# Performance work log

Hardware: AMD Instinct MI355X
Metric: run time of the kernel (lower is better)

The kernel has to match this reference:

```python
import jax, jax.numpy as jnp
import numpy as np

N, E, D, G, S, H = 100000, 1600000, 64, 1024, 4096, 128
BN_EPS = 1e-5


def setup_inputs() -> dict:
    key = jax.random.key(0)
    ks = jax.random.split(key, 24)
    x = jax.random.normal(ks[0], (N, D), jnp.float32)
    sid = jax.random.randint(ks[1], (N,), 0, S)
    x = x.at[:, 5].set(sid.astype(jnp.float32))  # column 5 holds integer substructure ids
    edge_index = jax.random.randint(ks[2], (2, E), 0, N, dtype=jnp.int32)
    batch = jnp.sort(jax.random.randint(ks[3], (N,), 0, G, dtype=jnp.int32))

    def lin(k, fan_in, shape):
        return jax.random.normal(k, shape, jnp.float32) / np.sqrt(fan_in)

    return {
        "x": x, "edge_index": edge_index, "batch": batch,
        # substructure attention net: Linear(D,64) -> tanh -> Linear(64,1,no bias)
        "w1": lin(ks[4], D, (D, 64)), "b1": jnp.zeros((64,), jnp.float32),
        "w2": lin(ks[5], 64, (64,)),
        "cw0": lin(ks[6], D + 1, (D + 1, H)), "cb0": jnp.zeros((H,), jnp.float32),
        "cw_rest": lin(ks[7], H, (3, H, H)), "cb_rest": jnp.zeros((3, H), jnp.float32),
        # BatchNorm1d (eval mode: running stats)
        "bn_gamma": jnp.ones((4, H), jnp.float32), "bn_beta": jnp.zeros((4, H), jnp.float32),
        "bn_mean": 0.1 * jax.random.normal(ks[8], (4, H), jnp.float32),
        "bn_var": jax.random.uniform(ks[9], (4, H), jnp.float32, 0.5, 1.5),
        # pred head: Linear(128,64) -> ELU -> Linear(64,1)
        "hw1": lin(ks[10], H, (H, 64)), "hb1": jnp.zeros((64,), jnp.float32),
        "hw2": lin(ks[11], 64, (64, 1)), "hb2": jnp.zeros((1,), jnp.float32),
    }


def _subst_attention(x, subst_ids, w1, b1, w2):
    ones = jnp.ones((x.shape[0],), x.dtype)
    cnt = jax.ops.segment_sum(ones, subst_ids, num_segments=S)
    sums = jax.ops.segment_sum(x, subst_ids, num_segments=S)
    means = sums / jnp.maximum(cnt, 1.0)[:, None]          # [S, D] per-substructure mean
    scores = jnp.tanh(means @ w1 + b1) @ w2                # [S]
    attn = jax.nn.softmax(scores, axis=0)                  # softmax over substructures
    return attn[subst_ids][:, None]                        # [N, 1] broadcast back to atoms


def _gcn(x, W, b, row, col, norm, n):
    h = x @ W                                              # [N, H]
    msg = h[row] * norm[:, None]                           # gather + scale  [E+N, H]
    return jax.ops.segment_sum(msg, col, num_segments=n) + b


def reference(x, edge_index, batch, w1, b1, w2, cw0, cb0, cw_rest, cb_rest,
              bn_gamma, bn_beta, bn_mean, bn_var, hw1, hb1, hw2, hb2):
    n = x.shape[0]
    subst_ids = jax.lax.stop_gradient(x[:, 5]).astype(jnp.int32)
    attn = _subst_attention(x, subst_ids, w1, b1, w2)
    h = jnp.concatenate([x, attn], axis=1)                 # [N, D+1]

    # add self loops, symmetric GCN normalization (as in PyG GCNConv)
    loops = jnp.arange(n, dtype=edge_index.dtype)
    row = jnp.concatenate([edge_index[0], loops])
    col = jnp.concatenate([edge_index[1], loops])
    deg = jax.ops.segment_sum(jnp.ones_like(row, dtype=h.dtype), col, num_segments=n)
    dinv = jax.lax.rsqrt(jnp.maximum(deg, 1.0))
    norm = dinv[row] * dinv[col]

    def bn(z, i):
        return (z - bn_mean[i]) * jax.lax.rsqrt(bn_var[i] + BN_EPS) * bn_gamma[i] + bn_beta[i]

    h = jax.nn.elu(bn(_gcn(h, cw0, cb0, row, col, norm, n), 0))
    for i in range(3):
        z = bn(_gcn(h, cw_rest[i], cb_rest[i], row, col, norm, n), i + 1)
        h = jax.nn.elu(z) if i < 2 else jax.nn.relu(z)

    # global mean pool over graphs
    gcnt = jax.ops.segment_sum(jnp.ones((n,), h.dtype), batch, num_segments=G)
    pooled = jax.ops.segment_sum(h, batch, num_segments=G) / jnp.maximum(gcnt, 1.0)[:, None]

    return jax.nn.elu(pooled @ hw1 + hb1) @ hw2 + hb2      # [G, 1]
```

## Files before the change

kernel.cpp:

```cpp
#include <hip/hip_runtime.h>
#include <math.h>

static constexpr int SS = 4096;
static constexpr int HH = 128;
static constexpr float EPS_BN = 1e-5f;

typedef __attribute__((ext_vector_type(8))) short bf16x8;
typedef __attribute__((ext_vector_type(4))) float f32x4;

__device__ inline unsigned short f2bf(float f) {
  unsigned int u = __float_as_uint(f);
  return (unsigned short)((u + 0x7fffu + ((u >> 16) & 1u)) >> 16);
}
__device__ inline float bflo(unsigned int u) { return __uint_as_float(u << 16); }
__device__ inline float bfhi(unsigned int u) { return __uint_as_float(u & 0xffff0000u); }


__global__ __launch_bounds__(256)
void gcn_front1(const int* __restrict__ col, int* __restrict__ fill, int* __restrict__ pos,
                const float* __restrict__ x, float* __restrict__ cnt, float* __restrict__ sums,
                int n, int e, int nbPos) {
  int b = blockIdx.x;
  int t = threadIdx.x;
  if (b < nbPos) {
    int i = b * 256 + t;
    if (i < e) pos[i] = atomicAdd(&fill[col[i]], 1);
    return;
  }
  b -= nbPos;
  {
    int node = b * 4 + (t >> 6);
    int lane = t & 63;
    if (node >= n) return;
    const float* xr = x + (size_t)node * 64;
    float v = xr[lane];
    int sid = (int)__shfl(v, 5, 64);
    if (lane == 0) atomicAdd(&cnt[sid], 1.0f);
    atomicAdd(&sums[(size_t)sid * 64 + lane], v);
  }
}


__global__ void gcn_scores(const float* __restrict__ sums, const float* __restrict__ cnt,
                           const float* __restrict__ w1, const float* __restrict__ b1,
                           const float* __restrict__ w2, float* __restrict__ scores) {
  int s = blockIdx.x * 4 + (threadIdx.x >> 6);
  int j = threadIdx.x & 63;
  float r = 1.0f / fmaxf(cnt[s], 1.0f);
  const float* ss = sums + (size_t)s * 64;
  float acc = b1[j];
  #pragma unroll 8
  for (int d = 0; d < 64; ++d) acc = fmaf(ss[d] * r, w1[d * 64 + j], acc);
  float t = tanhf(acc) * w2[j];
  #pragma unroll
  for (int off = 32; off; off >>= 1) t += __shfl_down(t, off, 64);
  if (j == 0) scores[s] = t;
}

__global__ void gcn_softmax(float* __restrict__ sc) {
  int t = threadIdx.x;
  int wid = t >> 6;
  float v[4]; float m = -INFINITY;
  for (int i = 0; i < 4; ++i) { v[i] = sc[t + i * 1024]; m = fmaxf(m, v[i]); }
  for (int off = 32; off; off >>= 1) m = fmaxf(m, __shfl_xor(m, off, 64));
  __shared__ float wmax[16];
  if ((t & 63) == 0) wmax[wid] = m;
  __syncthreads();
  if (t == 0) { float mm = wmax[0]; for (int i = 1; i < 16; ++i) mm = fmaxf(mm, wmax[i]); wmax[0] = mm; }
  __syncthreads();
  float M = wmax[0];
  float s = 0.f;
  for (int i = 0; i < 4; ++i) { v[i] = expf(v[i] - M); s += v[i]; }
  for (int off = 32; off; off >>= 1) s += __shfl_xor(s, off, 64);
  __shared__ float wsum[16];
  if ((t & 63) == 0) wsum[wid] = s;
  __syncthreads();
  if (t == 0) { float ts = 0.f; for (int i = 0; i < 16; ++i) ts += wsum[i]; wsum[0] = ts; }
  __syncthreads();
  float inv = 1.0f / wsum[0];
  for (int i = 0; i < 4; ++i) sc[t + i * 1024] = v[i] * inv;
}


__global__ void gcn_scan1(const int* __restrict__ fill, int* __restrict__ rowstart,
                          int* __restrict__ bsum, float* __restrict__ dinv, int n) {
  __shared__ int tmp[1024];
  int t = threadIdx.x; int g = blockIdx.x * 1024 + t;
  int v = (g < n) ? fill[g] : 0;
  if (g < n) dinv[g] = rsqrtf((float)v + 1.0f);
  tmp[t] = v; __syncthreads();
  for (int off = 1; off < 1024; off <<= 1) {
    int a = (t >= off) ? tmp[t - off] : 0; __syncthreads();
    tmp[t] += a; __syncthreads();
  }
  if (g < n) rowstart[g] = tmp[t] - v;
  if (t == 1023) bsum[blockIdx.x] = tmp[t];
}

__global__ void gcn_scan2(int* __restrict__ bsum, int nb) {
  __shared__ int tmp[128];
  int t = threadIdx.x;
  int v = (t < nb) ? bsum[t] : 0;
  tmp[t] = v; __syncthreads();
  for (int off = 1; off < 128; off <<= 1) {
    int a = (t >= off) ? tmp[t - off] : 0; __syncthreads();
    tmp[t] += a; __syncthreads();
  }
  if (t < nb) bsum[t] = tmp[t] - v;
}

__global__ void gcn_scan3(int* __restrict__ rowstart, const int* __restrict__ bsum, int n, int e) {
  int g = blockIdx.x * 1024 + threadIdx.x;
  if (g < n) rowstart[g] += bsum[blockIdx.x];
  if (g == 0) rowstart[n] = e;
}


__device__ void wpack_body(const float* __restrict__ W, unsigned short* __restrict__ out,
                           int nkc, int idx) {
  if (idx >= 8 * nkc * 64) return;
  int lane = idx & 63;
  int kc = (idx >> 6) % nkc;
  int nt = idx / (64 * nkc);
  int colc = nt * 16 + (lane & 15);
  int k0 = kc * 32 + (lane >> 4) * 8;
  unsigned int w[4];
  #pragma unroll
  for (int i = 0; i < 4; ++i) {
    unsigned short a = f2bf(W[(size_t)(k0 + 2 * i) * 128 + colc]);
    unsigned short b = f2bf(W[(size_t)(k0 + 2 * i + 1) * 128 + colc]);
    w[i] = (unsigned int)a | ((unsigned int)b << 16);
  }
  *(uint4*)&out[(size_t)idx * 8] = make_uint4(w[0], w[1], w[2], w[3]);
}

__global__ __launch_bounds__(256)
void gcn_front3(const float* __restrict__ x, const float* __restrict__ attn,
                float2* __restrict__ np,
                const int* __restrict__ row, const int* __restrict__ col,
                const int* __restrict__ pos, const int* __restrict__ rowstart,
                const float* __restrict__ dinv, int2* __restrict__ sedge,
                unsigned int* __restrict__ xh, const int* __restrict__ batch,
                int* __restrict__ gstart,
                const float* __restrict__ cw0, const float* __restrict__ cwr,
                unsigned short* __restrict__ wpk0, unsigned short* __restrict__ wpkr,
                const float* __restrict__ cb0, const float* __restrict__ cbr,
                const float* __restrict__ bng, const float* __restrict__ bnb,
                const float* __restrict__ bnm, const float* __restrict__ bnv,
                float* __restrict__ bnS, float* __restrict__ bnT,
                int n, int e, int G,
                int nbSc, int nbNp, int nbXb, int nbGb, int nbW0, int nbWr) {
  int b = blockIdx.x;
  int t = threadIdx.x;
  if (b < nbSc) {
    int i = b * 256 + t;
    if (i >= e) return;
    int c = col[i], r = row[i];
    sedge[rowstart[c] + pos[i]] = make_int2(r, __float_as_int(dinv[r] * dinv[c]));
    return;
  }
  b -= nbSc;
  if (b < nbNp) {
    int i = b * 256 + t;
    if (i >= n) return;
    int sid = (int)x[(size_t)i * 64 + 5];
    np[i] = make_float2((float)sid, attn[sid]);
    return;
  }
  b -= nbNp;
  if (b < nbXb) {
    int i = b * 256 + t;
    if (i >= n * 32) return;
    int pr = i & 31;
    float2 v = *(const float2*)&x[(size_t)(i >> 5) * 64 + pr * 2];
    if (pr == 2) v.y = 0.f;
    xh[i] = (unsigned int)f2bf(v.x) | ((unsigned int)f2bf(v.y) << 16);
    return;
  }
  b -= nbXb;
  if (b < nbGb) {
    int g = b * 256 + t;
    if (g > G) return;
    if (g == G) { gstart[G] = n; return; }
    int lo = 0, hi = n;
    while (lo < hi) { int mid = (lo + hi) >> 1; if (batch[mid] < g) lo = mid + 1; else hi = mid; }
    gstart[g] = lo;
    return;
  }
  b -= nbGb;
  if (b < nbW0) { wpack_body(cw0, wpk0, 2, b * 256 + t); return; }
  b -= nbW0;
  if (b < 3 * nbWr) {
    int l = b / nbWr, bb = b % nbWr;
    wpack_body(cwr + (size_t)l * HH * HH, wpkr + (size_t)l * 8 * 4 * 64 * 8, 4, bb * 256 + t);
    return;
  }
  b -= 3 * nbWr;
  {
    int i = b * 256 + t;
    if (i >= 512) return;
    int l = i >> 7, c = i & 127;
    float S = rsqrtf(bnv[i] + EPS_BN) * bng[i];
    float bias = (l == 0) ? cb0[c] : cbr[(l - 1) * 128 + c];
    bnS[i] = S;
    bnT[i] = fmaf(bias - bnm[i], S, bnb[i]);
  }
}


__global__ __launch_bounds__(256)
void gcn_layer_f(const unsigned short* __restrict__ hIn, const int2* __restrict__ sedge,
                 const int* __restrict__ rowstart, const float* __restrict__ dinv,
                 const unsigned short* __restrict__ Wpk,
                 const float* __restrict__ bnS, const float* __restrict__ bnT,
                 unsigned short* __restrict__ hOut, int relu, int n) {
  __shared__ unsigned short tile[4][16][136];
  int t = threadIdx.x;
  int wid = t >> 6, l = t & 63;
  int r = l & 15, kg = l >> 4;
  size_t row0w = (size_t)blockIdx.x * 64 + wid * 16;
  int noderaw = (int)row0w + r;
  bool valid = noderaw < n;
  int node = valid ? noderaw : n - 1;
  float di = dinv[node], d2 = di * di;
  const uint4* h4 = (const uint4*)hIn;
  float a[4][8];
  #pragma unroll
  for (int kc = 0; kc < 4; ++kc) {
    uint4 u = h4[(size_t)node * 16 + kc * 4 + kg];
    a[kc][0] = bflo(u.x) * d2; a[kc][1] = bfhi(u.x) * d2;
    a[kc][2] = bflo(u.y) * d2; a[kc][3] = bfhi(u.y) * d2;
    a[kc][4] = bflo(u.z) * d2; a[kc][5] = bfhi(u.z) * d2;
    a[kc][6] = bflo(u.w) * d2; a[kc][7] = bfhi(u.w) * d2;
  }
  int s_ = valid ? rowstart[node] : 0;
  int e_ = valid ? rowstart[node + 1] : 0;
  int j = s_;
  for (; j + 2 <= e_; j += 2) {
    int2 sA = sedge[j], sB = sedge[j + 1];
    float wA = __int_as_float(sA.y), wB = __int_as_float(sB.y);
    uint4 uA[4], uB[4];
    #pragma unroll
    for (int kc = 0; kc < 4; ++kc) uA[kc] = h4[(size_t)sA.x * 16 + kc * 4 + kg];
    #pragma unroll
    for (int kc = 0; kc < 4; ++kc) uB[kc] = h4[(size_t)sB.x * 16 + kc * 4 + kg];
    #pragma unroll
    for (int kc = 0; kc < 4; ++kc) {
      a[kc][0] = fmaf(bflo(uA[kc].x), wA, a[kc][0]); a[kc][1] = fmaf(bfhi(uA[kc].x), wA, a[kc][1]);
      a[kc][2] = fmaf(bflo(uA[kc].y), wA, a[kc][2]); a[kc][3] = fmaf(bfhi(uA[kc].y), wA, a[kc][3]);
      a[kc][4] = fmaf(bflo(uA[kc].z), wA, a[kc][4]); a[kc][5] = fmaf(bfhi(uA[kc].z), wA, a[kc][5]);
      a[kc][6] = fmaf(bflo(uA[kc].w), wA, a[kc][6]); a[kc][7] = fmaf(bfhi(uA[kc].w), wA, a[kc][7]);
    }
    #pragma unroll
    for (int kc = 0; kc < 4; ++kc) {
      a[kc][0] = fmaf(bflo(uB[kc].x), wB, a[kc][0]); a[kc][1] = fmaf(bfhi(uB[kc].x), wB, a[kc][1]);
      a[kc][2] = fmaf(bflo(uB[kc].y), wB, a[kc][2]); a[kc][3] = fmaf(bfhi(uB[kc].y), wB, a[kc][3]);
      a[kc][4] = fmaf(bflo(uB[kc].z), wB, a[kc][4]); a[kc][5] = fmaf(bfhi(uB[kc].z), wB, a[kc][5]);
      a[kc][6] = fmaf(bflo(uB[kc].w), wB, a[kc][6]); a[kc][7] = fmaf(bfhi(uB[kc].w), wB, a[kc][7]);
    }
  }
  if (j < e_) {
    int2 sA = sedge[j];
    float wA = __int_as_float(sA.y);
    #pragma unroll
    for (int kc = 0; kc < 4; ++kc) {
      uint4 u = h4[(size_t)sA.x * 16 + kc * 4 + kg];
      a[kc][0] = fmaf(bflo(u.x), wA, a[kc][0]); a[kc][1] = fmaf(bfhi(u.x), wA, a[kc][1]);
      a[kc][2] = fmaf(bflo(u.y), wA, a[kc][2]); a[kc][3] = fmaf(bfhi(u.y), wA, a[kc][3]);
      a[kc][4] = fmaf(bflo(u.z), wA, a[kc][4]); a[kc][5] = fmaf(bfhi(u.z), wA, a[kc][5]);
      a[kc][6] = fmaf(bflo(u.w), wA, a[kc][6]); a[kc][7] = fmaf(bfhi(u.w), wA, a[kc][7]);
    }
  }
  bf16x8 af[4];
  #pragma unroll
  for (int kc = 0; kc < 4; ++kc) {
    uint4 pk;
    pk.x = (unsigned)f2bf(a[kc][0]) | ((unsigned)f2bf(a[kc][1]) << 16);
    pk.y = (unsigned)f2bf(a[kc][2]) | ((unsigned)f2bf(a[kc][3]) << 16);
    pk.z = (unsigned)f2bf(a[kc][4]) | ((unsigned)f2bf(a[kc][5]) << 16);
    pk.w = (unsigned)f2bf(a[kc][6]) | ((unsigned)f2bf(a[kc][7]) << 16);
    af[kc] = *(bf16x8*)&pk;
  }
  f32x4 acc[8];
  #pragma unroll
  for (int nt = 0; nt < 8; ++nt) acc[nt] = (f32x4){0.f, 0.f, 0.f, 0.f};
  const unsigned short* wp = Wpk + (size_t)l * 8;
  #pragma unroll
  for (int kc = 0; kc < 4; ++kc) {
    bf16x8 bf[8];
    #pragma unroll
    for (int nt = 0; nt < 8; ++nt)
      bf[nt] = *(const bf16x8*)(wp + (size_t)(nt * 4 + kc) * 512);
    #pragma unroll
    for (int nt = 0; nt < 8; ++nt)
      acc[nt] = __builtin_amdgcn_mfma_f32_16x16x32_bf16(af[kc], bf[nt], acc[nt], 0, 0, 0);
  }
  int colb = l & 15, rb = kg * 4;
  #pragma unroll
  for (int nt = 0; nt < 8; ++nt) {
    int c = nt * 16 + colb;
    float S = bnS[c], T = bnT[c];
    #pragma unroll
    for (int jj = 0; jj < 4; ++jj) {
      float v = fmaf(acc[nt][jj], S, T);
      v = relu ? fmaxf(v, 0.f) : (v > 0.f ? v : expf(v) - 1.f);
      tile[wid][rb + jj][c] = f2bf(v);
    }
  }
  __syncthreads();
  #pragma unroll
  for (int i = 0; i < 4; ++i) {
    int m = i * 64 + l;
    int rr = m >> 4, chunk = m & 15;
    uint4 v = *(const uint4*)&tile[wid][rr][chunk * 8];
    *(uint4*)&hOut[(row0w + rr) * 128 + chunk * 8] = v;
  }
}


__global__ __launch_bounds__(256)
void gcn_layer0_f(const unsigned int* __restrict__ xh, const float2* __restrict__ np,
                  const int2* __restrict__ sedge, const int* __restrict__ rowstart,
                  const float* __restrict__ dinv, const unsigned short* __restrict__ Wpk0,
                  const float* __restrict__ cw0,
                  const float* __restrict__ bnS, const float* __restrict__ bnT,
                  unsigned short* __restrict__ hOut, int n) {
  __shared__ unsigned short tile[4][16][136];
  int t = threadIdx.x;
  int wid = t >> 6, l = t & 63;
  int r = l & 15, kg = l >> 4;
  size_t row0w = (size_t)blockIdx.x * 64 + wid * 16;
  int noderaw = (int)row0w + r;
  bool valid = noderaw < n;
  int node = valid ? noderaw : n - 1;
  float di = dinv[node], d2 = di * di;
  const uint4* x4 = (const uint4*)xh;
  float a[2][8];
  #pragma unroll
  for (int kc = 0; kc < 2; ++kc) {
    uint4 u = x4[(size_t)node * 8 + kc * 4 + kg];
    a[kc][0] = bflo(u.x) * d2; a[kc][1] = bfhi(u.x) * d2;
    a[kc][2] = bflo(u.y) * d2; a[kc][3] = bfhi(u.y) * d2;
    a[kc][4] = bflo(u.z) * d2; a[kc][5] = bfhi(u.z) * d2;
    a[kc][6] = bflo(u.w) * d2; a[kc][7] = bfhi(u.w) * d2;
  }
  float a5 = 0.f, a64 = 0.f;
  if (kg == 0) { float2 v = np[node]; a5 = d2 * v.x; a64 = d2 * v.y; }
  int s_ = valid ? rowstart[node] : 0;
  int e_ = valid ? rowstart[node + 1] : 0;
  int j = s_;
  for (; j + 2 <= e_; j += 2) {
    int2 sA = sedge[j], sB = sedge[j + 1];
    float wA = __int_as_float(sA.y), wB = __int_as_float(sB.y);
    uint4 uA[2], uB[2];
    #pragma unroll
    for (int kc = 0; kc < 2; ++kc) uA[kc] = x4[(size_t)sA.x * 8 + kc * 4 + kg];
    #pragma unroll
    for (int kc = 0; kc < 2; ++kc) uB[kc] = x4[(size_t)sB.x * 8 + kc * 4 + kg];
    float2 vA, vB;
    if (kg == 0) { vA = np[sA.x]; vB = np[sB.x]; }
    #pragma unroll
    for (int kc = 0; kc < 2; ++kc) {
      a[kc][0] = fmaf(bflo(uA[kc].x), wA, a[kc][0]); a[kc][1] = fmaf(bfhi(uA[kc].x), wA, a[kc][1]);
      a[kc][2] = fmaf(bflo(uA[kc].y), wA, a[kc][2]); a[kc][3] = fmaf(bfhi(uA[kc].y), wA, a[kc][3]);
      a[kc][4] = fmaf(bflo(uA[kc].z), wA, a[kc][4]); a[kc][5] = fmaf(bfhi(uA[kc].z), wA, a[kc][5]);
      a[kc][6] = fmaf(bflo(uA[kc].w), wA, a[kc][6]); a[kc][7] = fmaf(bfhi(uA[kc].w), wA, a[kc][7]);
      a[kc][0] = fmaf(bflo(uB[kc].x), wB, a[kc][0]); a[kc][1] = fmaf(bfhi(uB[kc].x), wB, a[kc][1]);
      a[kc][2] = fmaf(bflo(uB[kc].y), wB, a[kc][2]); a[kc][3] = fmaf(bfhi(uB[kc].y), wB, a[kc][3]);
      a[kc][4] = fmaf(bflo(uB[kc].z), wB, a[kc][4]); a[kc][5] = fmaf(bfhi(uB[kc].z), wB, a[kc][5]);
      a[kc][6] = fmaf(bflo(uB[kc].w), wB, a[kc][6]); a[kc][7] = fmaf(bfhi(uB[kc].w), wB, a[kc][7]);
    }
    if (kg == 0) {
      a5 = fmaf(vA.x, wA, a5); a64 = fmaf(vA.y, wA, a64);
      a5 = fmaf(vB.x, wB, a5); a64 = fmaf(vB.y, wB, a64);
    }
  }
  if (j < e_) {
    int2 sA = sedge[j];
    float wA = __int_as_float(sA.y);
    #pragma unroll
    for (int kc = 0; kc < 2; ++kc) {
      uint4 u = x4[(size_t)sA.x * 8 + kc * 4 + kg];
      a[kc][0] = fmaf(bflo(u.x), wA, a[kc][0]); a[kc][1] = fmaf(bfhi(u.x), wA, a[kc][1]);
      a[kc][2] = fmaf(bflo(u.y), wA, a[kc][2]); a[kc][3] = fmaf(bfhi(u.y), wA, a[kc][3]);
      a[kc][4] = fmaf(bflo(u.z), wA, a[kc][4]); a[kc][5] = fmaf(bfhi(u.z), wA, a[kc][5]);
      a[kc][6] = fmaf(bflo(u.w), wA, a[kc][6]); a[kc][7] = fmaf(bfhi(u.w), wA, a[kc][7]);
    }
    if (kg == 0) {
      float2 v = np[sA.x];
      a5 = fmaf(v.x, wA, a5); a64 = fmaf(v.y, wA, a64);
    }
  }
  bf16x8 af[2];
  #pragma unroll
  for (int kc = 0; kc < 2; ++kc) {
    uint4 pk;
    pk.x = (unsigned)f2bf(a[kc][0]) | ((unsigned)f2bf(a[kc][1]) << 16);
    pk.y = (unsigned)f2bf(a[kc][2]) | ((unsigned)f2bf(a[kc][3]) << 16);
    pk.z = (unsigned)f2bf(a[kc][4]) | ((unsigned)f2bf(a[kc][5]) << 16);
    pk.w = (unsigned)f2bf(a[kc][6]) | ((unsigned)f2bf(a[kc][7]) << 16);
    af[kc] = *(bf16x8*)&pk;
  }
  f32x4 acc[8];
  #pragma unroll
  for (int nt = 0; nt < 8; ++nt) acc[nt] = (f32x4){0.f, 0.f, 0.f, 0.f};
  const unsigned short* wp = Wpk0 + (size_t)l * 8;
  #pragma unroll
  for (int kc = 0; kc < 2; ++kc) {
    bf16x8 bf[8];
    #pragma unroll
    for (int nt = 0; nt < 8; ++nt)
      bf[nt] = *(const bf16x8*)(wp + (size_t)(nt * 2 + kc) * 512);
    #pragma unroll
    for (int nt = 0; nt < 8; ++nt)
      acc[nt] = __builtin_amdgcn_mfma_f32_16x16x32_bf16(af[kc], bf[nt], acc[nt], 0, 0, 0);
  }
  int colb = l & 15, rb = kg * 4;
  float2 ax[4];
  #pragma unroll
  for (int jj = 0; jj < 4; ++jj) {
    ax[jj].x = __shfl(a5, rb + jj, 64);
    ax[jj].y = __shfl(a64, rb + jj, 64);
  }
  #pragma unroll
  for (int nt = 0; nt < 8; ++nt) {
    int c = nt * 16 + colb;
    float w5 = cw0[5 * 128 + c], w64 = cw0[64 * 128 + c];
    float S = bnS[c], T = bnT[c];
    #pragma unroll
    for (int jj = 0; jj < 4; ++jj) {
      float z = acc[nt][jj] + ax[jj].x * w5 + ax[jj].y * w64;
      float v = fmaf(z, S, T);
      v = v > 0.f ? v : expf(v) - 1.f;
      tile[wid][rb + jj][c] = f2bf(v);
    }
  }
  __syncthreads();
  #pragma unroll
  for (int i = 0; i < 4; ++i) {
    int m = i * 64 + l;
    int rr = m >> 4, chunk = m & 15;
    uint4 v = *(const uint4*)&tile[wid][rr][chunk * 8];
    *(uint4*)&hOut[(row0w + rr) * 128 + chunk * 8] = v;
  }
}


__global__ __launch_bounds__(256)
void gcn_poolhead(const unsigned short* __restrict__ hB, const int* __restrict__ gstart,
                  const float* __restrict__ hw1, const float* __restrict__ hb1,
                  const float* __restrict__ hw2, const float* __restrict__ hb2,
                  float* __restrict__ out, int G) {
  __shared__ float pl[4][128];
  int wid = threadIdx.x >> 6, lane = threadIdx.x & 63;
  int g = blockIdx.x * 4 + wid;
  if (g >= G) return;
  int s = gstart[g], e = gstart[g + 1];
  const unsigned int* h32 = (const unsigned int*)hB;
  float ax = 0.f, ay = 0.f;
  int i = s;
  for (; i + 2 <= e; i += 2) {
    unsigned int u0 = h32[(size_t)i * 64 + lane];
    unsigned int u1 = h32[(size_t)(i + 1) * 64 + lane];
    ax += bflo(u0) + bflo(u1);
    ay += bfhi(u0) + bfhi(u1);
  }
  if (i < e) {
    unsigned int u = h32[(size_t)i * 64 + lane];
    ax += bflo(u); ay += bfhi(u);
  }
  float r = 1.0f / fmaxf((float)(e - s), 1.0f);
  pl[wid][lane * 2] = ax * r;
  pl[wid][lane * 2 + 1] = ay * r;
  float acc = hb1[lane];
  #pragma unroll 8
  for (int k = 0; k < 128; ++k) acc = fmaf(pl[wid][k], hw1[k * 64 + lane], acc);
  float t2 = acc > 0.f ? acc : expf(acc) - 1.f;
  t2 *= hw2[lane];
  #pragma unroll
  for (int off = 32; off; off >>= 1) t2 += __shfl_down(t2, off, 64);
  if (lane == 0) out[g] = t2 + hb2[0];
}


extern "C" void kernel_launch(void* const* d_in, const int* in_sizes, int n_in,
                              void* d_out, int out_size, void* d_ws, size_t ws_size,
                              hipStream_t stream) {
  const float* x   = (const float*)d_in[0];
  const int*   ei  = (const int*)d_in[1];
  const int*   batch = (const int*)d_in[2];
  const float* w1  = (const float*)d_in[3];
  const float* b1  = (const float*)d_in[4];
  const float* w2  = (const float*)d_in[5];
  const float* cw0 = (const float*)d_in[6];
  const float* cb0 = (const float*)d_in[7];
  const float* cwr = (const float*)d_in[8];
  const float* cbr = (const float*)d_in[9];
  const float* bng = (const float*)d_in[10];
  const float* bnb = (const float*)d_in[11];
  const float* bnm = (const float*)d_in[12];
  const float* bnv = (const float*)d_in[13];
  const float* hw1 = (const float*)d_in[14];
  const float* hb1 = (const float*)d_in[15];
  const float* hw2 = (const float*)d_in[16];
  const float* hb2 = (const float*)d_in[17];
  float* out = (float*)d_out;
  (void)n_in; (void)ws_size;

  const int n = in_sizes[0] / 64;
  const int e = in_sizes[1] / 2;
  const int G = out_size;
  const int* row = ei;
  const int* col = ei + e;
  const int nb128 = (n + 127) / 128;
  const int n_pad = nb128 * 128;

  char* p = (char*)d_ws;
  auto take = [&](size_t bytes) { char* r = p; p += (bytes + 255) & ~(size_t)255; return r; };
  float* cnt    = (float*)take((size_t)SS * 4);
  float* sums   = (float*)take((size_t)SS * 64 * 4);
  float* attn   = (float*)take((size_t)SS * 4);
  float* dinv   = (float*)take((size_t)n * 4);
  int*   rowst  = (int*)take(((size_t)n + 1) * 4);
  int*   fill   = (int*)take((size_t)n * 4);
  int*   pos    = (int*)take((size_t)e * 4);
  int*   bsum   = (int*)take(128 * 4);
  int*   gstart = (int*)take(((size_t)G + 1) * 4);
  int2*  sedge  = (int2*)take((size_t)e * 8);
  float2* np    = (float2*)take((size_t)n * 8);
  unsigned int* xh = (unsigned int*)take((size_t)n * 32 * 4);
  unsigned short* hP0 = (unsigned short*)take((size_t)n_pad * HH * 2);
  unsigned short* hP1 = (unsigned short*)take((size_t)n_pad * HH * 2);
  unsigned short* wpk0 = (unsigned short*)take((size_t)8 * 2 * 64 * 8 * 2);
  unsigned short* wpkr = (unsigned short*)take((size_t)3 * 8 * 4 * 64 * 8 * 2);
  float* bnS    = (float*)take(4 * 128 * 4);
  float* bnT    = (float*)take(4 * 128 * 4);

  hipMemsetAsync(cnt, 0, (size_t)SS * 4, stream);
  hipMemsetAsync(sums, 0, (size_t)SS * 64 * 4, stream);
  hipMemsetAsync(fill, 0, (size_t)n * 4, stream);

  int nbPos = (e + 255) / 256;
  int nbSub = (n + 3) / 4;
  gcn_front1<<<nbPos + nbSub, 256, 0, stream>>>(col, fill, pos, x, cnt, sums, n, e, nbPos);

  gcn_scores<<<SS / 4, 256, 0, stream>>>(sums, cnt, w1, b1, w2, attn);
  gcn_softmax<<<1, 1024, 0, stream>>>(attn);

  int nb = (n + 1023) / 1024;
  gcn_scan1<<<nb, 1024, 0, stream>>>(fill, rowst, bsum, dinv, n);
  gcn_scan2<<<1, 128, 0, stream>>>(bsum, nb);
  gcn_scan3<<<nb, 1024, 0, stream>>>(rowst, bsum, n, e);

  int nbSc = (e + 255) / 256;
  int nbNp = (n + 255) / 256;
  int nbXb = (n * 32 + 255) / 256;
  int nbGb = (G + 1 + 255) / 256;
  int nbW0 = 4, nbWr = 8, nbBnp = 2;
  int front3 = nbSc + nbNp + nbXb + nbGb + nbW0 + 3 * nbWr + nbBnp;
  gcn_front3<<<front3, 256, 0, stream>>>(x, attn, np, row, col, pos, rowst, dinv, sedge,
      xh, batch, gstart, cw0, cwr, wpk0, wpkr, cb0, cbr, bng, bnb, bnm, bnv, bnS, bnT,
      n, e, G, nbSc, nbNp, nbXb, nbGb, nbW0, nbWr);

  gcn_layer0_f<<<n_pad / 64, 256, 0, stream>>>(xh, np, sedge, rowst, dinv, wpk0, cw0,
      bnS, bnT, hP0, n);
  gcn_layer_f<<<n_pad / 64, 256, 0, stream>>>(hP0, sedge, rowst, dinv, wpkr,
      bnS + 128, bnT + 128, hP1, 0, n);
  gcn_layer_f<<<n_pad / 64, 256, 0, stream>>>(hP1, sedge, rowst, dinv,
      wpkr + (size_t)8 * 4 * 64 * 8, bnS + 256, bnT + 256, hP0, 0, n);
  gcn_layer_f<<<n_pad / 64, 256, 0, stream>>>(hP0, sedge, rowst, dinv,
      wpkr + (size_t)2 * 8 * 4 * 64 * 8, bnS + 384, bnT + 384, hP1, 1, n);

  gcn_poolhead<<<(G + 3) / 4, 256, 0, stream>>>(hP1, gstart, hw1, hb1, hw2, hb2, out, G);
}
```

Baseline: 608.9 us.

## Sort nodes by in-degree so GCN layer waves process similar-degree rows

Adds a degree histogram in the scan kernel, a bin scan and a scatter that build a permutation of nodes ordered by descending in-degree (capped at 63). The four GCN layer kernels map each tile row through this permutation and write results back to the original node row. The goal is to cut wavefront divergence in the per-lane edge-gather loop, since lanes in a wave now have similar edge counts. In exchange, writes and self-row reads become scattered, locality across neighbouring nodes is lost, and two small extra kernels are launched.

```diff
diff --git a/kernel.cpp b/kernel.cpp
--- a/kernel.cpp
+++ b/kernel.cpp
@@ -83,18 +83,23 @@
 
 
 __global__ void gcn_scan1(const int* __restrict__ fill, int* __restrict__ rowstart,
-                          int* __restrict__ bsum, float* __restrict__ dinv, int n) {
+                          int* __restrict__ bsum, float* __restrict__ dinv,
+                          int* __restrict__ bh, int n) {
   __shared__ int tmp[1024];
+  __shared__ int hist[64];
   int t = threadIdx.x; int g = blockIdx.x * 1024 + t;
+  if (t < 64) hist[t] = 0;
   int v = (g < n) ? fill[g] : 0;
   if (g < n) dinv[g] = rsqrtf((float)v + 1.0f);
   tmp[t] = v; __syncthreads();
+  if (g < n) atomicAdd(&hist[v > 63 ? 63 : v], 1);
   for (int off = 1; off < 1024; off <<= 1) {
     int a = (t >= off) ? tmp[t - off] : 0; __syncthreads();
     tmp[t] += a; __syncthreads();
   }
   if (g < n) rowstart[g] = tmp[t] - v;
   if (t == 1023) bsum[blockIdx.x] = tmp[t];
+  if (t < 64) bh[blockIdx.x * 64 + t] = hist[t];
 }
 
 __global__ void gcn_scan2(int* __restrict__ bsum, int nb) {
@@ -113,6 +118,38 @@
   int g = blockIdx.x * 1024 + threadIdx.x;
   if (g < n) rowstart[g] += bsum[blockIdx.x];
   if (g == 0) rowstart[n] = e;
+}
+
+
+__global__ void gcn_dscan(int* __restrict__ bh, int* __restrict__ binbase, int nbh) {
+  int t = threadIdx.x;
+  int tot = 0;
+  for (int b = 0; b < nbh; ++b) {
+    int v = bh[b * 64 + t];
+    bh[b * 64 + t] = tot;
+    tot += v;
+  }
+  int s = tot;
+  #pragma unroll
+  for (int off = 1; off < 64; off <<= 1) {
+    int u = __shfl_up(s, off, 64);
+    if (t >= off) s += u;
+  }
+  binbase[t] = s - tot;
+}
+
+__global__ void gcn_dscatter(const int* __restrict__ fill, const int* __restrict__ bh,
+                             const int* __restrict__ binbase, int* __restrict__ perm, int n) {
+  __shared__ int h[64];
+  int t = threadIdx.x;
+  if (t < 64) h[t] = bh[blockIdx.x * 64 + t] + binbase[t];
+  __syncthreads();
+  int i = blockIdx.x * 1024 + t;
+  if (i < n) {
+    int d = fill[i]; if (d > 63) d = 63;
+    int p = atomicAdd(&h[d], 1);
+    perm[n - 1 - p] = i;
+  }
 }
 
 
@@ -211,6 +248,7 @@
 __global__ __launch_bounds__(256)
 void gcn_layer_f(const unsigned short* __restrict__ hIn, const int2* __restrict__ sedge,
                  const int* __restrict__ rowstart, const float* __restrict__ dinv,
+                 const int* __restrict__ perm,
                  const unsigned short* __restrict__ Wpk,
                  const float* __restrict__ bnS, const float* __restrict__ bnT,
                  unsigned short* __restrict__ hOut, int relu, int n) {
@@ -219,22 +257,24 @@
   int wid = t >> 6, l = t & 63;
   int r = l & 15, kg = l >> 4;
   size_t row0w = (size_t)blockIdx.x * 64 + wid * 16;
-  int noderaw = (int)row0w + r;
-  bool valid = noderaw < n;
-  int node = valid ? noderaw : n - 1;
-  float di = dinv[node], d2 = di * di;
+  int tileRow = (int)row0w + r;
+  bool valid = tileRow < n;
+  int pidx = valid ? tileRow : 0;
+  int node = valid ? perm[pidx] : tileRow;
+  int nrd = valid ? node : 0;
+  float di = dinv[nrd], d2 = di * di;
   const uint4* h4 = (const uint4*)hIn;
   float a[4][8];
   #pragma unroll
   for (int kc = 0; kc < 4; ++kc) {
-    uint4 u = h4[(size_t)node * 16 + kc * 4 + kg];
+    uint4 u = h4[(size_t)nrd * 16 + kc * 4 + kg];
     a[kc][0] = bflo(u.x) * d2; a[kc][1] = bfhi(u.x) * d2;
     a[kc][2] = bflo(u.y) * d2; a[kc][3] = bfhi(u.y) * d2;
     a[kc][4] = bflo(u.z) * d2; a[kc][5] = bfhi(u.z) * d2;
     a[kc][6] = bflo(u.w) * d2; a[kc][7] = bfhi(u.w) * d2;
   }
-  int s_ = valid ? rowstart[node] : 0;
-  int e_ = valid ? rowstart[node + 1] : 0;
+  int s_ = valid ? rowstart[nrd] : 0;
+  int e_ = valid ? rowstart[nrd + 1] : 0;
   int j = s_;
   for (; j + 2 <= e_; j += 2) {
     int2 sA = sedge[j], sB = sedge[j + 1];
@@ -307,13 +347,15 @@
       tile[wid][rb + jj][c] = f2bf(v);
     }
   }
+  __shared__ int srow[4][16];
+  if (kg == 0) srow[wid][r] = valid ? node : tileRow;
   __syncthreads();
   #pragma unroll
   for (int i = 0; i < 4; ++i) {
     int m = i * 64 + l;
     int rr = m >> 4, chunk = m & 15;
     uint4 v = *(const uint4*)&tile[wid][rr][chunk * 8];
-    *(uint4*)&hOut[(row0w + rr) * 128 + chunk * 8] = v;
+    *(uint4*)&hOut[(size_t)srow[wid][rr] * 128 + chunk * 8] = v;
   }
 }
 
@@ -321,7 +363,8 @@
 __global__ __launch_bounds__(256)
 void gcn_layer0_f(const unsigned int* __restrict__ xh, const float2* __restrict__ np,
                   const int2* __restrict__ sedge, const int* __restrict__ rowstart,
-                  const float* __restrict__ dinv, const unsigned short* __restrict__ Wpk0,
+                  const float* __restrict__ dinv, const int* __restrict__ perm,
+                  const unsigned short* __restrict__ Wpk0,
                   const float* __restrict__ cw0,
                   const float* __restrict__ bnS, const float* __restrict__ bnT,
                   unsigned short* __restrict__ hOut, int n) {
@@ -330,24 +373,26 @@
   int wid = t >> 6, l = t & 63;
   int r = l & 15, kg = l >> 4;
   size_t row0w = (size_t)blockIdx.x * 64 + wid * 16;
-  int noderaw = (int)row0w + r;
-  bool valid = noderaw < n;
-  int node = valid ? noderaw : n - 1;
-  float di = dinv[node], d2 = di * di;
+  int tileRow = (int)row0w + r;
+  bool valid = tileRow < n;
+  int pidx = valid ? tileRow : 0;
+  int node = valid ? perm[pidx] : tileRow;
+  int nrd = valid ? node : 0;
+  float di = dinv[nrd], d2 = di * di;
   const uint4* x4 = (const uint4*)xh;
   float a[2][8];
   #pragma unroll
   for (int kc = 0; kc < 2; ++kc) {
-    uint4 u = x4[(size_t)node * 8 + kc * 4 + kg];
+    uint4 u = x4[(size_t)nrd * 8 + kc * 4 + kg];
     a[kc][0] = bflo(u.x) * d2; a[kc][1] = bfhi(u.x) * d2;
     a[kc][2] = bflo(u.y) * d2; a[kc][3] = bfhi(u.y) * d2;
     a[kc][4] = bflo(u.z) * d2; a[kc][5] = bfhi(u.z) * d2;
     a[kc][6] = bflo(u.w) * d2; a[kc][7] = bfhi(u.w) * d2;
   }
   float a5 = 0.f, a64 = 0.f;
-  if (kg == 0) { float2 v = np[node]; a5 = d2 * v.x; a64 = d2 * v.y; }
-  int s_ = valid ? rowstart[node] : 0;
-  int e_ = valid ? rowstart[node + 1] : 0;
+  if (kg == 0) { float2 v = np[nrd]; a5 = d2 * v.x; a64 = d2 * v.y; }
+  int s_ = valid ? rowstart[nrd] : 0;
+  int e_ = valid ? rowstart[nrd + 1] : 0;
   int j = s_;
   for (; j + 2 <= e_; j += 2) {
     int2 sA = sedge[j], sB = sedge[j + 1];
@@ -435,13 +480,15 @@
       tile[wid][rb + jj][c] = f2bf(v);
     }
   }
+  __shared__ int srow[4][16];
+  if (kg == 0) srow[wid][r] = valid ? node : tileRow;
   __syncthreads();
   #pragma unroll
   for (int i = 0; i < 4; ++i) {
     int m = i * 64 + l;
     int rr = m >> 4, chunk = m & 15;
     uint4 v = *(const uint4*)&tile[wid][rr][chunk * 8];
-    *(uint4*)&hOut[(row0w + rr) * 128 + chunk * 8] = v;
+    *(uint4*)&hOut[(size_t)srow[wid][rr] * 128 + chunk * 8] = v;
   }
 }
 
@@ -514,6 +561,7 @@
   const int* col = ei + e;
   const int nb128 = (n + 127) / 128;
   const int n_pad = nb128 * 128;
+  const int nb1 = (n + 1023) / 1024;
 
   char* p = (char*)d_ws;
   auto take = [&](size_t bytes) { char* r = p; p += (bytes + 255) & ~(size_t)255; return r; };
@@ -525,6 +573,9 @@
   int*   fill   = (int*)take((size_t)n * 4);
   int*   pos    = (int*)take((size_t)e * 4);
   int*   bsum   = (int*)take(128 * 4);
+  int*   bh     = (int*)take((size_t)nb1 * 64 * 4);
+  int*   binbase= (int*)take(64 * 4);
+  int*   perm   = (int*)take((size_t)n * 4);
   int*   gstart = (int*)take(((size_t)G + 1) * 4);
   int2*  sedge  = (int2*)take((size_t)e * 8);
   float2* np    = (float2*)take((size_t)n * 8);
@@ -547,10 +598,11 @@
   gcn_scores<<<SS / 4, 256, 0, stream>>>(sums, cnt, w1, b1, w2, attn);
   gcn_softmax<<<1, 1024, 0, stream>>>(attn);
 
-  int nb = (n + 1023) / 1024;
-  gcn_scan1<<<nb, 1024, 0, stream>>>(fill, rowst, bsum, dinv, n);
-  gcn_scan2<<<1, 128, 0, stream>>>(bsum, nb);
-  gcn_scan3<<<nb, 1024, 0, stream>>>(rowst, bsum, n, e);
+  gcn_scan1<<<nb1, 1024, 0, stream>>>(fill, rowst, bsum, dinv, bh, n);
+  gcn_scan2<<<1, 128, 0, stream>>>(bsum, nb1);
+  gcn_dscan<<<1, 64, 0, stream>>>(bh, binbase, nb1);
+  gcn_scan3<<<nb1, 1024, 0, stream>>>(rowst, bsum, n, e);
+  gcn_dscatter<<<nb1, 1024, 0, stream>>>(fill, bh, binbase, perm, n);
 
   int nbSc = (e + 255) / 256;
   int nbNp = (n + 255) / 256;
@@ -562,13 +614,13 @@
       xh, batch, gstart, cw0, cwr, wpk0, wpkr, cb0, cbr, bng, bnb, bnm, bnv, bnS, bnT,
       n, e, G, nbSc, nbNp, nbXb, nbGb, nbW0, nbWr);
 
-  gcn_layer0_f<<<n_pad / 64, 256, 0, stream>>>(xh, np, sedge, rowst, dinv, wpk0, cw0,
+  gcn_layer0_f<<<n_pad / 64, 256, 0, stream>>>(xh, np, sedge, rowst, dinv, perm, wpk0, cw0,
       bnS, bnT, hP0, n);
-  gcn_layer_f<<<n_pad / 64, 256, 0, stream>>>(hP0, sedge, rowst, dinv, wpkr,
+  gcn_layer_f<<<n_pad / 64, 256, 0, stream>>>(hP0, sedge, rowst, dinv, perm, wpkr,
       bnS + 128, bnT + 128, hP1, 0, n);
-  gcn_layer_f<<<n_pad / 64, 256, 0, stream>>>(hP1, sedge, rowst, dinv,
+  gcn_layer_f<<<n_pad / 64, 256, 0, stream>>>(hP1, sedge, rowst, dinv, perm,
       wpkr + (size_t)8 * 4 * 64 * 8, bnS + 256, bnT + 256, hP0, 0, n);
-  gcn_layer_f<<<n_pad / 64, 256, 0, stream>>>(hP0, sedge, rowst, dinv,
+  gcn_layer_f<<<n_pad / 64, 256, 0, stream>>>(hP0, sedge, rowst, dinv, perm,
       wpkr + (size_t)2 * 8 * 4 * 64 * 8, bnS + 384, bnT + 384, hP1, 1, n);
 
   gcn_poolhead<<<(G + 3) / 4, 256, 0, stream>>>(hP1, gstart, hw1, hb1, hw2, hb2, out, G);
```

After: 606.6 us. About the same (-0.4%).
